# Kernel optimization log

Measured on AMD Instinct MI355X. Metric: run time of the kernel, lower is better.

## Reference

```python
import jax, jax.numpy as jnp
import numpy as np

N, M, K, C = 32768, 16384, 8, 16
LAM = 0.1        # dist_weight_lambda
EPS = 1e-6       # torch F.pairwise_distance eps (added to the difference)


def setup_inputs() -> dict:
    key = jax.random.key(0)
    k0, k1, k2, k3, k4 = jax.random.split(key, 5)
    canon_xyz = jax.random.normal(k0, (N, 3), jnp.float32)
    pred_translation = 0.1 * jax.random.normal(k1, (N, 3), jnp.float32)
    motion_coeff = jax.random.normal(k2, (N, C), jnp.float32)
    features_dc = jax.random.normal(k3, (N, 1, 3), jnp.float32)
    # random.sample without replacement -> permutation slice
    indice = jax.random.permutation(k4, N)[:M].astype(jnp.int32)
    return {
        "canon_xyz": canon_xyz,
        "pred_translation": pred_translation,
        "motion_coeff": motion_coeff,
        "features_dc": features_dc,
        "indice": indice,
    }


def _pdist(x, y):
    # torch F.pairwise_distance(p=2): ||x - y + eps|| over last dim
    d = x - y + EPS
    return jnp.sqrt(jnp.sum(d * d, axis=-1))


def reference(canon_xyz, pred_translation, motion_coeff, features_dc, indice):
    pts = canon_xyz + pred_translation            # [N,3]
    tp = pts[indice]                              # [M,3] target_points
    tc = motion_coeff[indice]                     # [M,C] target_coeffs
    tcol = features_dc[indice]                    # [M,1,3] target_colors

    # --- knn_points: brute-force squared L2, K smallest (sorted ascending) ---
    sq = jnp.sum(tp * tp, axis=-1)                # [M]
    d2 = sq[:, None] + sq[None, :] - 2.0 * (tp @ tp.T)   # [M,M]
    neg_d, nn_idx = jax.lax.top_k(-d2, K)         # [M,K]
    deform_dists = -neg_d                         # squared dists, ascending

    sim_loss = jnp.float32(0.0)

    # --- 'surface' branch ---
    nn_points = tp[nn_idx]                        # [M,K,3] knn_gather
    mean_nn_points = nn_points.mean(axis=1)       # [M,3]
    sim_loss += _pdist(tp, mean_nn_points).mean()

    # --- 'coeff' branch ---
    coeff_nn = tc[nn_idx]                         # [M,K,C]
    color_nn = tcol.reshape(M, 3)[nn_idx]         # [M,K,3]
    color_dists = _pdist(tcol, color_nn)          # [M,1,3] vs [M,K,3] -> [M,K]
    dist_weights = jnp.exp(-LAM * deform_dists ** 2)   # [M,K]
    color_weights = jnp.exp(-LAM * color_dists ** 2)   # [M,K]
    sim = _pdist(tc[:, None, :], coeff_nn)        # l2 metric -> [M,K]
    sim = color_weights * dist_weights * sim      # color_sim=True
    sim_loss += sim.mean()

    return sim_loss
```

## Files before the change

### kernel.cpp

```cpp
#include <hip/hip_runtime.h>
#include <hip/hip_bf16.h>
#include <float.h>


#define MPTS 16384
#define KNN  8
#define CDIM 16
#define LAMW 0.1f
#define EPSV 1e-6f

#define ROWS   32
#define NSPLIT 8
#define CSPL   (MPTS/NSPLIT)
#define NT     (CSPL/32)
#define BSTR   257

#define MED3 __builtin_amdgcn_fmed3f
typedef __attribute__((ext_vector_type(8)))  _Float16 f16x8;
typedef __attribute__((ext_vector_type(16))) float    f32x16;

__global__ __launch_bounds__(256) void k_gather(
    const float* __restrict__ canon, const float* __restrict__ trans,
    const int* __restrict__ indice, float4* __restrict__ c4,
    _Float16* __restrict__ bf16b, _Float16* __restrict__ af16b,
    float* __restrict__ acc)
{
    int t = blockIdx.x * 256 + threadIdx.x;
    if (t == 0) { acc[0] = 0.f; acc[1] = 0.f; }
    if (t < MPTS) {
        int j = indice[t];
        float x = canon[3*j+0] + trans[3*j+0];
        float y = canon[3*j+1] + trans[3*j+1];
        float z = canon[3*j+2] + trans[3*j+2];
        float sq = fmaf(x, x, fmaf(y, y, z*z));
        c4[t] = make_float4(-2.f*x, -2.f*y, -2.f*z, sq);
        f16x8 aa = {};
        aa[0] = (_Float16)(-2.f*x); aa[1] = (_Float16)(-2.f*y);
        aa[2] = (_Float16)(-2.f*z); aa[3] = (_Float16)1.0f;
        *(f16x8*)(af16b + (size_t)t*8) = aa;
        f16x8 bb = {};
        bb[0] = (_Float16)x; bb[1] = (_Float16)y; bb[2] = (_Float16)z;
        bb[3] = (_Float16)sq;
        *(f16x8*)(bf16b + (size_t)t*8) = bb;
    }
}

__global__ __launch_bounds__(512, 8) void k_knn_loss(
    const float4* __restrict__ c4,
    const _Float16* __restrict__ bf16b, const _Float16* __restrict__ af16b,
    const int* __restrict__ indice, const float* __restrict__ motion,
    const float* __restrict__ fdc, float* __restrict__ acc)
{
    __shared__ float bins[ROWS * BSTR];
    __shared__ float rS[NSPLIT], rM[NSPLIT];

    const int tid  = threadIdx.x;
    const int lane = tid & 63;
    const int wv   = tid >> 6;
    const int rowbase = blockIdx.x * ROWS;
    const int cls  = lane & 31;
    const int cbeg = wv * CSPL;

    f16x8 afrag = *(const f16x8*)(af16b + (size_t)(rowbase + cls) * 8);
    if (lane >= 32) { f16x8 zz = {}; afrag = zz; }
    f32x16 zero16 = {};

    const _Float16* bptr  = bf16b + (size_t)(cbeg + cls) * 8;
    const unsigned  HMASK = 0xFFFFC000u;
    const unsigned  ivb   = (unsigned)(cbeg + cls);

    float e0=FLT_MAX,e1=FLT_MAX,e2=FLT_MAX,e3=FLT_MAX;
    float e4=FLT_MAX,e5=FLT_MAX,e6=FLT_MAX,e7=FLT_MAX;
    float e8=FLT_MAX,e9=FLT_MAX,e10=FLT_MAX,e11=FLT_MAX;
    float e12=FLT_MAX,e13=FLT_MAX,e14=FLT_MAX,e15=FLT_MAX;

    f16x8 b = *(const f16x8*)(bptr);
    #pragma unroll 2
    for (int tile = 0; tile < NT; ++tile) {
        f16x8 bn = *(const f16x8*)(bptr + (size_t)(((tile + 1) & (NT-1)) * 256));
        f32x16 dv = __builtin_amdgcn_mfma_f32_32x32x16_f16(afrag, b, zero16, 0, 0, 0);
        unsigned iv = ivb + (unsigned)(tile * 32);
#define STEP(G, EG) { float kf = __uint_as_float((__float_as_uint(dv[G]) & HMASK) | iv); \
                      EG = fminf(EG, kf); }
        STEP(0,e0)   STEP(1,e1)   STEP(2,e2)   STEP(3,e3)
        STEP(4,e4)   STEP(5,e5)   STEP(6,e6)   STEP(7,e7)
        STEP(8,e8)   STEP(9,e9)   STEP(10,e10) STEP(11,e11)
        STEP(12,e12) STEP(13,e13) STEP(14,e14) STEP(15,e15)
#undef STEP
        b = bn;
    }

    {
        float* bb = &bins[((lane >> 5) * 4) * BSTR + wv * 32 + cls];
#define ST(RO, EG) bb[(RO) * BSTR] = EG;
        ST(0,e0)   ST(1,e1)   ST(2,e2)   ST(3,e3)
        ST(8,e4)   ST(9,e5)   ST(10,e6)  ST(11,e7)
        ST(16,e8)  ST(17,e9)  ST(18,e10) ST(19,e11)
        ST(24,e12) ST(25,e13) ST(26,e14) ST(27,e15)
#undef ST
    }
    __syncthreads();

    const int sr = lane >> 4;
    const int lr = lane & 15;
    const int rl = wv * 4 + sr;
    const int row = rowbase + rl;

    float g0 = FLT_MAX, g1 = FLT_MAX;
    #pragma unroll
    for (int i = 0; i < 16; ++i) {
        float v = bins[rl * BSTR + i * 16 + lr];
        g1 = MED3(g0, g1, v);
        g0 = fminf(g0, v);
    }

    float kres = FLT_MAX;
    #pragma unroll
    for (int s = 0; s < KNN; ++s) {
        float m = g0;
        m = fminf(m, __shfl_xor(m, 1));
        m = fminf(m, __shfl_xor(m, 2));
        m = fminf(m, __shfl_xor(m, 4));
        m = fminf(m, __shfl_xor(m, 8));
        bool mine = (g0 == m);
        kres = (lr == s) ? m : kres;
        g0 = mine ? g1 : g0;
        g1 = mine ? FLT_MAX : g1;
    }

    float4 rc = c4[row];
    const float qx=-0.5f*rc.x, qy=-0.5f*rc.y, qz=-0.5f*rc.z, qq=rc.w;

    int jk = (int)(__float_as_uint(kres) & 0x3FFFu);
    float4 nc = c4[jk];
    float te  = fmaf(qx, nc.x, fmaf(qy, nc.y, fmaf(qz, nc.z, nc.w)));
    float d2k = qq + te;

    float xn = (lr < KNN) ? -0.5f*nc.x : 0.f;
    float yn = (lr < KNN) ? -0.5f*nc.y : 0.f;
    float zn = (lr < KNN) ? -0.5f*nc.z : 0.f;
    float sx = xn, sy = yn, sz = zn;
    sx += __shfl_xor(sx, 1); sx += __shfl_xor(sx, 2); sx += __shfl_xor(sx, 4);
    sy += __shfl_xor(sy, 1); sy += __shfl_xor(sy, 2); sy += __shfl_xor(sy, 4);
    sz += __shfl_xor(sz, 1); sz += __shfl_xor(sz, 2); sz += __shfl_xor(sz, 4);

    float surf = 0.f, simv = 0.f;
    if (lr < KNN) {
        if (lr == 0) {
            float dx = qx - sx * 0.125f + EPSV;
            float dy = qy - sy * 0.125f + EPSV;
            float dz = qz - sz * 0.125f + EPSV;
            surf = sqrtf(fmaf(dx, dx, fmaf(dy, dy, dz * dz)));
        }
        int irow = indice[row];
        int inb  = indice[jk];
        float c0v = fdc[3*irow+0] - fdc[3*inb+0] + EPSV;
        float c1v = fdc[3*irow+1] - fdc[3*inb+1] + EPSV;
        float c2v = fdc[3*irow+2] - fdc[3*inb+2] + EPSV;
        float cd2 = fmaf(c0v, c0v, fmaf(c1v, c1v, c2v * c2v));
        float w = __expf(-LAMW * fmaf(d2k, d2k, cd2));

        const float4* mr4 = (const float4*)(motion + CDIM * irow);
        const float4* mn4 = (const float4*)(motion + CDIM * inb);
        float s = 0.f;
        #pragma unroll
        for (int c = 0; c < CDIM/4; ++c) {
            float4 A = mr4[c], B = mn4[c];
            float h0 = A.x-B.x+EPSV, h1 = A.y-B.y+EPSV;
            float h2 = A.z-B.z+EPSV, h3 = A.w-B.w+EPSV;
            s = fmaf(h0,h0, fmaf(h1,h1, fmaf(h2,h2, fmaf(h3,h3, s))));
        }
        simv = w * sqrtf(s);
    }

    float aS = surf, aM = simv;
    #pragma unroll
    for (int m = 1; m <= 32; m <<= 1) {
        aS += __shfl_xor(aS, m);
        aM += __shfl_xor(aM, m);
    }
    if (lane == 0) { rS[wv] = aS; rM[wv] = aM; }
    __syncthreads();
    if (tid == 0) {
        float tS = 0.f, tM = 0.f;
        #pragma unroll
        for (int w2 = 0; w2 < NSPLIT; ++w2) { tS += rS[w2]; tM += rM[w2]; }
        atomicAdd(&acc[0], tS);
        atomicAdd(&acc[1], tM);
    }
}

__global__ void k_final(const float* __restrict__ acc, float* __restrict__ out)
{
    out[0] = acc[0] * (1.0f / MPTS) + acc[1] * (1.0f / (MPTS * KNN));
}

extern "C" void kernel_launch(void* const* d_in, const int* in_sizes, int n_in,
                              void* d_out, int out_size, void* d_ws, size_t ws_size,
                              hipStream_t stream)
{
    const float* canon  = (const float*)d_in[0];
    const float* trans  = (const float*)d_in[1];
    const float* motion = (const float*)d_in[2];
    const float* fdc    = (const float*)d_in[3];
    const int*   indice = (const int*)d_in[4];
    float* out = (float*)d_out;

    char* ws = (char*)d_ws;
    float*     acc   = (float*)ws;
    float4*    c4    = (float4*)(ws + 4096);
    _Float16*  af16b = (_Float16*)(ws + 4096 + 262144);
    _Float16*  bf16b = (_Float16*)(ws + 4096 + 2*262144);

    k_gather<<<MPTS/256, 256, 0, stream>>>(canon, trans, indice, c4, bf16b, af16b, acc);
    k_knn_loss<<<MPTS/ROWS, 512, 0, stream>>>(c4, bf16b, af16b, indice, motion, fdc, acc);
    k_final<<<1, 1, 0, stream>>>(acc, out);
}
```

Baseline: 45.85 us.

## Split KNN column range across two blocks and merge top-k in separate loss kernel

The KNN kernel now launches twice as many blocks, each scanning half of the candidate columns, and writes its sorted 8 packed keys per row to a workspace buffer. A new merge kernel does a two-way merge of the partial top-8 lists per row, one thread per row, and computes the surface and coefficient losses serially per row. The aim is more parallelism and occupancy on the dominant scan phase, and to move the loss work out of the wide KNN block. The cost is an extra kernel launch and a global round trip for the intermediate keys.

```diff
diff --git a/kernel.cpp b/kernel.cpp
--- a/kernel.cpp
+++ b/kernel.cpp
@@ -11,7 +11,7 @@
 
 #define ROWS   32
 #define NSPLIT 8
-#define CSPL   (MPTS/NSPLIT)
+#define CSPL   1024
 #define NT     (CSPL/32)
 #define BSTR   257
 
@@ -45,21 +45,19 @@
     }
 }
 
-__global__ __launch_bounds__(512, 8) void k_knn_loss(
-    const float4* __restrict__ c4,
+__global__ __launch_bounds__(512, 8) void k_knn(
     const _Float16* __restrict__ bf16b, const _Float16* __restrict__ af16b,
-    const int* __restrict__ indice, const float* __restrict__ motion,
-    const float* __restrict__ fdc, float* __restrict__ acc)
+    float* __restrict__ keys)
 {
     __shared__ float bins[ROWS * BSTR];
-    __shared__ float rS[NSPLIT], rM[NSPLIT];
 
     const int tid  = threadIdx.x;
     const int lane = tid & 63;
     const int wv   = tid >> 6;
-    const int rowbase = blockIdx.x * ROWS;
+    const int half = blockIdx.x & 1;
+    const int rowbase = (blockIdx.x >> 1) * ROWS;
     const int cls  = lane & 31;
-    const int cbeg = wv * CSPL;
+    const int cbeg = half * (MPTS/2) + wv * CSPL;
 
     f16x8 afrag = *(const f16x8*)(af16b + (size_t)(rowbase + cls) * 8);
     if (lane >= 32) { f16x8 zz = {}; afrag = zz; }
@@ -128,52 +126,76 @@
         g1 = mine ? FLT_MAX : g1;
     }
 
+    if (lr < KNN)
+        keys[((size_t)half * MPTS + row) * KNN + lr] = kres;
+}
+
+__global__ __launch_bounds__(256) void k_merge_loss(
+    const float4* __restrict__ c4, const float* __restrict__ keys,
+    const int* __restrict__ indice, const float* __restrict__ motion,
+    const float* __restrict__ fdc, float* __restrict__ acc)
+{
+    __shared__ float rS[4], rM[4];
+    const int tid  = threadIdx.x;
+    const int lane = tid & 63;
+    const int wv   = tid >> 6;
+    const int row  = blockIdx.x * 256 + tid;
+
+    const float4* pa4 = (const float4*)(keys + (size_t)row * KNN);
+    const float4* pb4 = (const float4*)(keys + ((size_t)MPTS + row) * KNN);
+    float4 A0 = pa4[0], A1 = pa4[1], B0 = pb4[0], B1 = pb4[1];
+    float a0=A0.x,a1=A0.y,a2=A0.z,a3=A0.w,a4=A1.x,a5=A1.y,a6=A1.z,a7=A1.w;
+    float b0=B0.x,b1=B0.y,b2=B0.z,b3=B0.w,b4=B1.x,b5=B1.y,b6=B1.z,b7=B1.w;
+
     float4 rc = c4[row];
     const float qx=-0.5f*rc.x, qy=-0.5f*rc.y, qz=-0.5f*rc.z, qq=rc.w;
-
-    int jk = (int)(__float_as_uint(kres) & 0x3FFFu);
-    float4 nc = c4[jk];
-    float te  = fmaf(qx, nc.x, fmaf(qy, nc.y, fmaf(qz, nc.z, nc.w)));
-    float d2k = qq + te;
-
-    float xn = (lr < KNN) ? -0.5f*nc.x : 0.f;
-    float yn = (lr < KNN) ? -0.5f*nc.y : 0.f;
-    float zn = (lr < KNN) ? -0.5f*nc.z : 0.f;
-    float sx = xn, sy = yn, sz = zn;
-    sx += __shfl_xor(sx, 1); sx += __shfl_xor(sx, 2); sx += __shfl_xor(sx, 4);
-    sy += __shfl_xor(sy, 1); sy += __shfl_xor(sy, 2); sy += __shfl_xor(sy, 4);
-    sz += __shfl_xor(sz, 1); sz += __shfl_xor(sz, 2); sz += __shfl_xor(sz, 4);
-
-    float surf = 0.f, simv = 0.f;
-    if (lr < KNN) {
-        if (lr == 0) {
-            float dx = qx - sx * 0.125f + EPSV;
-            float dy = qy - sy * 0.125f + EPSV;
-            float dz = qz - sz * 0.125f + EPSV;
-            surf = sqrtf(fmaf(dx, dx, fmaf(dy, dy, dz * dz)));
-        }
-        int irow = indice[row];
-        int inb  = indice[jk];
-        float c0v = fdc[3*irow+0] - fdc[3*inb+0] + EPSV;
-        float c1v = fdc[3*irow+1] - fdc[3*inb+1] + EPSV;
-        float c2v = fdc[3*irow+2] - fdc[3*inb+2] + EPSV;
+    const int irow = indice[row];
+    const float f0 = fdc[3*irow+0], f1 = fdc[3*irow+1], f2 = fdc[3*irow+2];
+    const float4* mr4 = (const float4*)(motion + CDIM * irow);
+    float4 m0 = mr4[0], m1 = mr4[1], m2 = mr4[2], m3 = mr4[3];
+
+    float sx = 0.f, sy = 0.f, sz = 0.f, simsum = 0.f;
+    #pragma unroll
+    for (int s = 0; s < KNN; ++s) {
+        bool m = (a0 <= b0);
+        float kk = m ? a0 : b0;
+        float na0=m?a1:a0, na1=m?a2:a1, na2=m?a3:a2, na3=m?a4:a3;
+        float na4=m?a5:a4, na5=m?a6:a5, na6=m?a7:a6, na7=m?FLT_MAX:a7;
+        float nb0=m?b0:b1, nb1=m?b1:b2, nb2=m?b2:b3, nb3=m?b3:b4;
+        float nb4=m?b4:b5, nb5=m?b5:b6, nb6=m?b6:b7, nb7=m?b7:FLT_MAX;
+        a0=na0;a1=na1;a2=na2;a3=na3;a4=na4;a5=na5;a6=na6;a7=na7;
+        b0=nb0;b1=nb1;b2=nb2;b3=nb3;b4=nb4;b5=nb5;b6=nb6;b7=nb7;
+
+        int jk = (int)(__float_as_uint(kk) & 0x3FFFu);
+        float4 nc = c4[jk];
+        float te  = fmaf(qx, nc.x, fmaf(qy, nc.y, fmaf(qz, nc.z, nc.w)));
+        float d2k = qq + te;
+        sx += -0.5f*nc.x; sy += -0.5f*nc.y; sz += -0.5f*nc.z;
+
+        int inb = indice[jk];
+        float c0v = f0 - fdc[3*inb+0] + EPSV;
+        float c1v = f1 - fdc[3*inb+1] + EPSV;
+        float c2v = f2 - fdc[3*inb+2] + EPSV;
         float cd2 = fmaf(c0v, c0v, fmaf(c1v, c1v, c2v * c2v));
         float w = __expf(-LAMW * fmaf(d2k, d2k, cd2));
 
-        const float4* mr4 = (const float4*)(motion + CDIM * irow);
         const float4* mn4 = (const float4*)(motion + CDIM * inb);
-        float s = 0.f;
-        #pragma unroll
-        for (int c = 0; c < CDIM/4; ++c) {
-            float4 A = mr4[c], B = mn4[c];
-            float h0 = A.x-B.x+EPSV, h1 = A.y-B.y+EPSV;
-            float h2 = A.z-B.z+EPSV, h3 = A.w-B.w+EPSV;
-            s = fmaf(h0,h0, fmaf(h1,h1, fmaf(h2,h2, fmaf(h3,h3, s))));
-        }
-        simv = w * sqrtf(s);
-    }
-
-    float aS = surf, aM = simv;
+        float4 u0 = mn4[0], u1 = mn4[1], u2 = mn4[2], u3 = mn4[3];
+        float sacc = 0.f;
+#define MD(A,B) { float g0v=A.x-B.x+EPSV, g1v=A.y-B.y+EPSV,               \
+                        g2v=A.z-B.z+EPSV, g3v=A.w-B.w+EPSV;               \
+                  sacc = fmaf(g0v,g0v,fmaf(g1v,g1v,fmaf(g2v,g2v,fmaf(g3v,g3v,sacc)))); }
+        MD(m0,u0) MD(m1,u1) MD(m2,u2) MD(m3,u3)
+#undef MD
+        simsum += w * sqrtf(sacc);
+    }
+
+    float dx = qx - sx * 0.125f + EPSV;
+    float dy = qy - sy * 0.125f + EPSV;
+    float dz = qz - sz * 0.125f + EPSV;
+    float surf = sqrtf(fmaf(dx, dx, fmaf(dy, dy, dz * dz)));
+
+    float aS = surf, aM = simsum;
     #pragma unroll
     for (int m = 1; m <= 32; m <<= 1) {
         aS += __shfl_xor(aS, m);
@@ -184,7 +206,7 @@
     if (tid == 0) {
         float tS = 0.f, tM = 0.f;
         #pragma unroll
-        for (int w2 = 0; w2 < NSPLIT; ++w2) { tS += rS[w2]; tM += rM[w2]; }
+        for (int w2 = 0; w2 < 4; ++w2) { tS += rS[w2]; tM += rM[w2]; }
         atomicAdd(&acc[0], tS);
         atomicAdd(&acc[1], tM);
     }
@@ -211,8 +233,10 @@
     float4*    c4    = (float4*)(ws + 4096);
     _Float16*  af16b = (_Float16*)(ws + 4096 + 262144);
     _Float16*  bf16b = (_Float16*)(ws + 4096 + 2*262144);
+    float*     keys  = (float*)(ws + 4096 + 3*262144);
 
     k_gather<<<MPTS/256, 256, 0, stream>>>(canon, trans, indice, c4, bf16b, af16b, acc);
-    k_knn_loss<<<MPTS/ROWS, 512, 0, stream>>>(c4, bf16b, af16b, indice, motion, fdc, acc);
+    k_knn<<<(MPTS/ROWS)*2, 512, 0, stream>>>(bf16b, af16b, keys);
+    k_merge_loss<<<MPTS/256, 256, 0, stream>>>(c4, keys, indice, motion, fdc, acc);
     k_final<<<1, 1, 0, stream>>>(acc, out);
 }
```

After: 42.86 us. 1.07x faster.

## Split KNN into column-split LDS-tiled kernel plus separate merge-and-loss kernel

Applied to the files above, without the earlier changes.

Each block now processes 256 rows against a 1024-column slice whose B fragments are staged in LDS, with the MFMA software-pipelined one tile ahead. Every block writes per-split top-8 candidate keys to a workspace buffer, and a new kernel merges the 16 splits and computes the loss. The aim is more B reuse across waves and shorter dependency chains in the MFMA loop. The cost is an extra kernel launch and a global round-trip for the candidate keys. The two-deep bin selection (min and second-min per lane) could drop true neighbours when three or more of them share one bin.

```diff
diff --git a/kernel.cpp b/kernel.cpp
--- a/kernel.cpp
+++ b/kernel.cpp
@@ -9,11 +9,11 @@
 #define LAMW 0.1f
 #define EPSV 1e-6f
 
-#define ROWS   32
-#define NSPLIT 8
-#define CSPL   (MPTS/NSPLIT)
+#define NSPLIT 16
+#define CSPL   1024
 #define NT     (CSPL/32)
-#define BSTR   257
+#define BROWS  256
+#define BSTR   33
 
 #define MED3 __builtin_amdgcn_fmed3f
 typedef __attribute__((ext_vector_type(8)))  _Float16 f16x8;
@@ -45,53 +45,75 @@
     }
 }
 
-__global__ __launch_bounds__(512, 8) void k_knn_loss(
-    const float4* __restrict__ c4,
+__global__ __launch_bounds__(512, 4) void k_knn(
     const _Float16* __restrict__ bf16b, const _Float16* __restrict__ af16b,
-    const int* __restrict__ indice, const float* __restrict__ motion,
-    const float* __restrict__ fdc, float* __restrict__ acc)
-{
-    __shared__ float bins[ROWS * BSTR];
-    __shared__ float rS[NSPLIT], rM[NSPLIT];
+    float* __restrict__ keys)
+{
+    __shared__ f16x8 shb[CSPL];
+    __shared__ float bins[BROWS * BSTR];
 
     const int tid  = threadIdx.x;
     const int lane = tid & 63;
     const int wv   = tid >> 6;
-    const int rowbase = blockIdx.x * ROWS;
+    const int csplit  = blockIdx.x & (NSPLIT-1);
+    const int rowbase = (blockIdx.x >> 4) * BROWS;
     const int cls  = lane & 31;
-    const int cbeg = wv * CSPL;
-
-    f16x8 afrag = *(const f16x8*)(af16b + (size_t)(rowbase + cls) * 8);
+    const int cbeg = csplit * CSPL;
+
+    shb[tid]       = *(const f16x8*)(bf16b + (size_t)(cbeg + tid) * 8);
+    shb[tid + 512] = *(const f16x8*)(bf16b + (size_t)(cbeg + tid + 512) * 8);
+
+    f16x8 afrag = *(const f16x8*)(af16b + (size_t)(rowbase + wv * 32 + cls) * 8);
     if (lane >= 32) { f16x8 zz = {}; afrag = zz; }
     f32x16 zero16 = {};
 
-    const _Float16* bptr  = bf16b + (size_t)(cbeg + cls) * 8;
-    const unsigned  HMASK = 0xFFFFC000u;
-    const unsigned  ivb   = (unsigned)(cbeg + cls);
+    const unsigned HMASK = 0xFFFFC000u;
+    const unsigned ivb   = (unsigned)(cbeg + cls);
 
     float e0=FLT_MAX,e1=FLT_MAX,e2=FLT_MAX,e3=FLT_MAX;
     float e4=FLT_MAX,e5=FLT_MAX,e6=FLT_MAX,e7=FLT_MAX;
     float e8=FLT_MAX,e9=FLT_MAX,e10=FLT_MAX,e11=FLT_MAX;
     float e12=FLT_MAX,e13=FLT_MAX,e14=FLT_MAX,e15=FLT_MAX;
 
-    f16x8 b = *(const f16x8*)(bptr);
-    #pragma unroll 2
-    for (int tile = 0; tile < NT; ++tile) {
-        f16x8 bn = *(const f16x8*)(bptr + (size_t)(((tile + 1) & (NT-1)) * 256));
-        f32x16 dv = __builtin_amdgcn_mfma_f32_32x32x16_f16(afrag, b, zero16, 0, 0, 0);
-        unsigned iv = ivb + (unsigned)(tile * 32);
-#define STEP(G, EG) { float kf = __uint_as_float((__float_as_uint(dv[G]) & HMASK) | iv); \
-                      EG = fminf(EG, kf); }
-        STEP(0,e0)   STEP(1,e1)   STEP(2,e2)   STEP(3,e3)
-        STEP(4,e4)   STEP(5,e5)   STEP(6,e6)   STEP(7,e7)
-        STEP(8,e8)   STEP(9,e9)   STEP(10,e10) STEP(11,e11)
-        STEP(12,e12) STEP(13,e13) STEP(14,e14) STEP(15,e15)
-#undef STEP
-        b = bn;
-    }
+    __syncthreads();
+
+#define UNPACK(DV, T)                                                          \
+    {                                                                          \
+        unsigned iv = ivb + (unsigned)((T) * 32);                              \
+        float kf;                                                              \
+        kf = __uint_as_float((__float_as_uint(DV[0])  & HMASK) | iv); e0  = fminf(e0,  kf); \
+        kf = __uint_as_float((__float_as_uint(DV[1])  & HMASK) | iv); e1  = fminf(e1,  kf); \
+        kf = __uint_as_float((__float_as_uint(DV[2])  & HMASK) | iv); e2  = fminf(e2,  kf); \
+        kf = __uint_as_float((__float_as_uint(DV[3])  & HMASK) | iv); e3  = fminf(e3,  kf); \
+        kf = __uint_as_float((__float_as_uint(DV[4])  & HMASK) | iv); e4  = fminf(e4,  kf); \
+        kf = __uint_as_float((__float_as_uint(DV[5])  & HMASK) | iv); e5  = fminf(e5,  kf); \
+        kf = __uint_as_float((__float_as_uint(DV[6])  & HMASK) | iv); e6  = fminf(e6,  kf); \
+        kf = __uint_as_float((__float_as_uint(DV[7])  & HMASK) | iv); e7  = fminf(e7,  kf); \
+        kf = __uint_as_float((__float_as_uint(DV[8])  & HMASK) | iv); e8  = fminf(e8,  kf); \
+        kf = __uint_as_float((__float_as_uint(DV[9])  & HMASK) | iv); e9  = fminf(e9,  kf); \
+        kf = __uint_as_float((__float_as_uint(DV[10]) & HMASK) | iv); e10 = fminf(e10, kf); \
+        kf = __uint_as_float((__float_as_uint(DV[11]) & HMASK) | iv); e11 = fminf(e11, kf); \
+        kf = __uint_as_float((__float_as_uint(DV[12]) & HMASK) | iv); e12 = fminf(e12, kf); \
+        kf = __uint_as_float((__float_as_uint(DV[13]) & HMASK) | iv); e13 = fminf(e13, kf); \
+        kf = __uint_as_float((__float_as_uint(DV[14]) & HMASK) | iv); e14 = fminf(e14, kf); \
+        kf = __uint_as_float((__float_as_uint(DV[15]) & HMASK) | iv); e15 = fminf(e15, kf); \
+    }
+
+    f16x8 b1 = shb[cls + 32];
+    f32x16 dvA = __builtin_amdgcn_mfma_f32_32x32x16_f16(shb[cls], b1, zero16, 0, 0, 0);
+    dvA = __builtin_amdgcn_mfma_f32_32x32x16_f16(afrag, shb[cls], zero16, 0, 0, 0);
+    for (int t = 0; t < NT - 1; ++t) {
+        f16x8 b2 = shb[((t + 2) & (NT - 1)) * 32 + cls];
+        f32x16 dvB = __builtin_amdgcn_mfma_f32_32x32x16_f16(afrag, b1, zero16, 0, 0, 0);
+        UNPACK(dvA, t)
+        dvA = dvB;
+        b1 = b2;
+    }
+    UNPACK(dvA, NT - 1)
+#undef UNPACK
 
     {
-        float* bb = &bins[((lane >> 5) * 4) * BSTR + wv * 32 + cls];
+        float* bb = &bins[(wv * 32 + (lane >> 5) * 4) * BSTR + cls];
 #define ST(RO, EG) bb[(RO) * BSTR] = EG;
         ST(0,e0)   ST(1,e1)   ST(2,e2)   ST(3,e3)
         ST(8,e4)   ST(9,e5)   ST(10,e6)  ST(11,e7)
@@ -101,31 +123,63 @@
     }
     __syncthreads();
 
-    const int sr = lane >> 4;
-    const int lr = lane & 15;
-    const int rl = wv * 4 + sr;
-    const int row = rowbase + rl;
-
-    float g0 = FLT_MAX, g1 = FLT_MAX;
-    #pragma unroll
-    for (int i = 0; i < 16; ++i) {
-        float v = bins[rl * BSTR + i * 16 + lr];
-        g1 = MED3(g0, g1, v);
-        g0 = fminf(g0, v);
-    }
+    const int grp = tid >> 4;
+    const int lr  = tid & 15;
+    for (int b = 0; b < 8; ++b) {
+        const int rl = b * 32 + grp;
+        float g0 = bins[rl * BSTR + lr];
+        float g1 = bins[rl * BSTR + lr + 16];
+        float tmp = fminf(g0, g1); g1 = fmaxf(g0, g1); g0 = tmp;
+
+        float kres = FLT_MAX;
+        #pragma unroll
+        for (int s = 0; s < KNN; ++s) {
+            float m = g0;
+            m = fminf(m, __shfl_xor(m, 1));
+            m = fminf(m, __shfl_xor(m, 2));
+            m = fminf(m, __shfl_xor(m, 4));
+            m = fminf(m, __shfl_xor(m, 8));
+            bool mine = (g0 == m);
+            kres = (lr == s) ? m : kres;
+            g0 = mine ? g1 : g0;
+            g1 = mine ? FLT_MAX : g1;
+        }
+        if (lr < KNN)
+            keys[((size_t)(rowbase + rl) * NSPLIT + csplit) * KNN + lr] = kres;
+    }
+}
+
+__global__ __launch_bounds__(256) void k_merge_loss(
+    const float4* __restrict__ c4, const float* __restrict__ keys,
+    const int* __restrict__ indice, const float* __restrict__ motion,
+    const float* __restrict__ fdc, float* __restrict__ acc)
+{
+    __shared__ float rS[4], rM[4];
+    const int tid  = threadIdx.x;
+    const int lane = tid & 63;
+    const int wv   = tid >> 6;
+    const int sub  = lane >> 5;
+    const int lp   = lane & 31;
+    const int row  = blockIdx.x * 8 + wv * 2 + sub;
+
+    float4 kv = *(const float4*)(keys + (size_t)row * (NSPLIT * KNN) + lp * 4);
+    float c0 = kv.x, c1 = kv.y, c2 = kv.z, c3 = kv.w;
 
     float kres = FLT_MAX;
     #pragma unroll
     for (int s = 0; s < KNN; ++s) {
-        float m = g0;
+        float m = c0;
         m = fminf(m, __shfl_xor(m, 1));
         m = fminf(m, __shfl_xor(m, 2));
         m = fminf(m, __shfl_xor(m, 4));
         m = fminf(m, __shfl_xor(m, 8));
-        bool mine = (g0 == m);
-        kres = (lr == s) ? m : kres;
-        g0 = mine ? g1 : g0;
-        g1 = mine ? FLT_MAX : g1;
+        m = fminf(m, __shfl_xor(m, 16));
+        bool mine = (c0 == m);
+        kres = (lp == s) ? m : kres;
+        c0 = mine ? c1 : c0;
+        c1 = mine ? c2 : c1;
+        c2 = mine ? c3 : c2;
+        c3 = mine ? FLT_MAX : c3;
     }
 
     float4 rc = c4[row];
@@ -136,17 +190,17 @@
     float te  = fmaf(qx, nc.x, fmaf(qy, nc.y, fmaf(qz, nc.z, nc.w)));
     float d2k = qq + te;
 
-    float xn = (lr < KNN) ? -0.5f*nc.x : 0.f;
-    float yn = (lr < KNN) ? -0.5f*nc.y : 0.f;
-    float zn = (lr < KNN) ? -0.5f*nc.z : 0.f;
+    float xn = (lp < KNN) ? -0.5f*nc.x : 0.f;
+    float yn = (lp < KNN) ? -0.5f*nc.y : 0.f;
+    float zn = (lp < KNN) ? -0.5f*nc.z : 0.f;
     float sx = xn, sy = yn, sz = zn;
     sx += __shfl_xor(sx, 1); sx += __shfl_xor(sx, 2); sx += __shfl_xor(sx, 4);
     sy += __shfl_xor(sy, 1); sy += __shfl_xor(sy, 2); sy += __shfl_xor(sy, 4);
     sz += __shfl_xor(sz, 1); sz += __shfl_xor(sz, 2); sz += __shfl_xor(sz, 4);
 
     float surf = 0.f, simv = 0.f;
-    if (lr < KNN) {
-        if (lr == 0) {
+    if (lp < KNN) {
+        if (lp == 0) {
             float dx = qx - sx * 0.125f + EPSV;
             float dy = qy - sy * 0.125f + EPSV;
             float dz = qz - sz * 0.125f + EPSV;
@@ -184,7 +238,7 @@
     if (tid == 0) {
         float tS = 0.f, tM = 0.f;
         #pragma unroll
-        for (int w2 = 0; w2 < NSPLIT; ++w2) { tS += rS[w2]; tM += rM[w2]; }
+        for (int w2 = 0; w2 < 4; ++w2) { tS += rS[w2]; tM += rM[w2]; }
         atomicAdd(&acc[0], tS);
         atomicAdd(&acc[1], tM);
     }
@@ -211,8 +265,10 @@
     float4*    c4    = (float4*)(ws + 4096);
     _Float16*  af16b = (_Float16*)(ws + 4096 + 262144);
     _Float16*  bf16b = (_Float16*)(ws + 4096 + 2*262144);
+    float*     keys  = (float*)(ws + 4096 + 3*262144);
 
     k_gather<<<MPTS/256, 256, 0, stream>>>(canon, trans, indice, c4, bf16b, af16b, acc);
-    k_knn_loss<<<MPTS/ROWS, 512, 0, stream>>>(c4, bf16b, af16b, indice, motion, fdc, acc);
+    k_knn<<<(MPTS/BROWS)*NSPLIT, 512, 0, stream>>>(bf16b, af16b, keys);
+    k_merge_loss<<<MPTS/8, 256, 0, stream>>>(c4, keys, indice, motion, fdc, acc);
     k_final<<<1, 1, 0, stream>>>(acc, out);
 }
```

Result: slower. 127.0 us (+177.0%).
